# Optimization experiments

Measured on AMD Instinct MI355X. Metric: run time of the kernel, lower is better.

## Reference

```python
import jax, jax.numpy as jnp
import numpy as np

B, T = 256, 50
N_ITEMS = 100000
EMB = 256      # embedding
KBD = 128      # KBembedding == MN_dims
HID = 256      # layers[0] == layers[-1]
OUT = 256      # out_dim
NF = 10        # MN_nfactors == n_r


def setup_inputs() -> dict:
    key = jax.random.key(0)
    ks = jax.random.split(key, 18)
    s = 0.05
    return {
        "X": jax.random.randint(ks[0], (B, T), 0, N_ITEMS),
        "E": jax.random.normal(ks[1], (N_ITEMS, EMB), jnp.float32) * s,
        "KBE": jax.random.normal(ks[2], (N_ITEMS, KBD), jnp.float32) * s,
        "r_matrix": jax.random.normal(ks[3], (NF, KBD), jnp.float32) * s,
        "W_ih": jax.random.normal(ks[4], (3 * HID, EMB), jnp.float32) * s,
        "W_hh": jax.random.normal(ks[5], (3 * HID, HID), jnp.float32) * s,
        "b_ih": jnp.zeros((3 * HID,), jnp.float32),
        "b_hh": jnp.zeros((3 * HID,), jnp.float32),
        "MNu_W": jax.random.normal(ks[6], (KBD, HID), jnp.float32) * s,
        "MNu_b": jnp.zeros((KBD,), jnp.float32),
        "MNu2_W": jax.random.normal(ks[7], (HID, KBD + HID), jnp.float32) * s,
        "MNu2_b": jnp.zeros((HID,), jnp.float32),
        "MNea_W": jax.random.normal(ks[8], (KBD, KBD), jnp.float32) * s,
        "MNea_b": jnp.zeros((KBD,), jnp.float32),
        "mlp1_W": jax.random.normal(ks[9], (OUT, HID), jnp.float32) * s,
        "mlp1_b": jnp.zeros((OUT,), jnp.float32),
        "mlp2_W": jax.random.normal(ks[10], (OUT, EMB + KBD), jnp.float32) * s,
        "mlp2_b": jnp.zeros((OUT,), jnp.float32),
    }


def _gru_cell(x, h, W_ih, W_hh, b_ih, b_hh):
    # PyTorch GRUCell: gates stacked [r, z, n] along dim 0 of weights
    gi = x @ W_ih.T + b_ih
    gh = h @ W_hh.T + b_hh
    ir, iz, inn = jnp.split(gi, 3, axis=-1)
    hr, hz, hn = jnp.split(gh, 3, axis=-1)
    r = jax.nn.sigmoid(ir + hr)
    z = jax.nn.sigmoid(iz + hz)
    n = jnp.tanh(inn + r * hn)
    return (1.0 - z) * n + z * h


def reference(X, E, KBE, r_matrix, W_ih, W_hh, b_ih, b_hh,
              MNu_W, MNu_b, MNu2_W, MNu2_b, MNea_W, MNea_b,
              mlp1_W, mlp1_b, mlp2_W, mlp2_b):
    Bv, Tv = X.shape
    Em = E.at[0].set(0.0)     # mask row 0 of E
    KBm = KBE.at[0].set(0.0)  # mask row 0 of KBE
    Sx = Em[X]                # (B, T, EMB)
    KBItem = KBm[X]           # (B, T, KBD)

    def step(carry, xs):
        h, MN, y_sum = carry
        x_t, kb_t = xs                      # (B, EMB), (B, KBD)
        h = _gru_cell(x_t, h, W_ih, W_hh, b_ih, b_hh)
        y = h                                # dropout p=0 -> identity
        # gated memory write
        EA = jnp.tanh(kb_t @ MNea_W.T + MNea_b)          # (B, KBD)
        EA = EA[:, None, :] + r_matrix                    # (B, NF, KBD)
        gate = jax.nn.sigmoid(jnp.sum(MN * EA, axis=-1, keepdims=True))  # (B, NF, 1)
        MN = MN * (1.0 - gate) + EA * gate
        # attention read
        U = jnp.tanh(y @ MNu_W.T + MNu_b)                 # (B, KBD)
        AW = jax.nn.softmax(U @ r_matrix.T, axis=1)       # (B, NF)
        AC = jnp.einsum('bfd,bf->bd', MN, AW)             # (B, KBD)
        Ut = jnp.tanh(jnp.concatenate([y, AC], axis=-1) @ MNu2_W.T + MNu2_b)  # (B, HID)
        y_out = jnp.tanh(Ut @ mlp1_W.T + mlp1_b)          # (B, OUT)
        return (h, MN, y_sum + y_out), None

    init = (jnp.zeros((Bv, HID), Sx.dtype),
            jnp.zeros((Bv, NF, KBD), Sx.dtype),
            jnp.zeros((Bv, OUT), Sx.dtype))
    xs = (jnp.swapaxes(Sx, 0, 1), jnp.swapaxes(KBItem, 0, 1))  # (T, B, *)
    (h, MN, y_sum), _ = jax.lax.scan(step, init, xs)
    y = y_sum / Tv

    MergeE = jnp.concatenate([E, KBE], axis=1).at[0].set(0.0)  # (N, EMB+KBD)
    Sy = jnp.tanh(MergeE @ mlp2_W.T + mlp2_b)                  # (N, OUT)
    scores = jax.nn.log_softmax(y @ Sy.T, axis=1)              # (B, N)
    return scores, y
```

## Files before the change

kernel.cpp:

```cpp
#include <hip/hip_runtime.h>

typedef _Float16 f16;
typedef _Float16 f16x8 __attribute__((ext_vector_type(8)));
typedef float f32x4 __attribute__((ext_vector_type(4)));

#define MFMA16(a,b,c) __builtin_amdgcn_mfma_f32_16x16x32_f16(a,b,c,0,0,0)

#define NITEMS 100000
#define NBLK4  1563

#define OFF_WIH   0u
#define OFF_WHH   393216u
#define OFF_MNU   786432u
#define OFF_MNU2  851968u
#define OFF_MNEA  1048576u
#define OFF_MLP1  1081344u
#define OFF_MLP2  1212416u
#define OFF_GI    1409024u
#define OFF_TV    21069824u
#define OFF_MN    24346624u
#define OFF_YALL  57114624u
#define OFF_SY    66945024u
#define OFF_Y16   118407168u
#define OFF_PMAX  118538240u
#define OFF_PSUM  120176640u
#define OFF_LSE   121815040u

__device__ __forceinline__ float sigm(float x) { return 1.f / (1.f + __expf(-x)); }
__device__ __forceinline__ float tanh_fast(float x) {
  return 1.f - 2.f / (1.f + __expf(2.f * x));
}

__global__ __launch_bounds__(256) void k_pack(
    const float* s0, const float* s1, const float* s2, const float* s3,
    const float* s4, const float* s5, const float* s6, f16* base)
{
  int fid = blockIdx.x * 256 + threadIdx.x;
  const float* src; f16* dst; int K, f;
  if (fid < 24576)      { src = s0; dst = base;          K = 256; f = fid; }
  else if (fid < 49152) { src = s1; dst = base + 196608; K = 256; f = fid - 24576; }
  else if (fid < 53248) { src = s2; dst = base + 393216; K = 256; f = fid - 49152; }
  else if (fid < 65536) { src = s3; dst = base + 425984; K = 384; f = fid - 53248; }
  else if (fid < 67584) { src = s4; dst = base + 524288; K = 128; f = fid - 65536; }
  else if (fid < 75776) { src = s5; dst = base + 540672; K = 256; f = fid - 67584; }
  else                  { src = s6; dst = base + 606208; K = 384; f = fid - 75776; }
  int lane = f & 63, t2 = f >> 6, KS = K >> 5;
  int ks = t2 % KS, nt = t2 / KS;
  int row = nt * 16 + (lane & 15), col = ks * 32 + ((lane >> 4) << 3);
  const float* sp = src + (size_t)row * K + col;
  f16x8 v;
  #pragma unroll
  for (int j = 0; j < 8; j++) v[j] = (f16)sp[j];
  *(f16x8*)(dst + (size_t)f * 8) = v;
}

__global__ __launch_bounds__(512) void k_giea(
    const int* __restrict__ X, const float* __restrict__ E,
    const f16* __restrict__ Wih_p, const float* __restrict__ bih, f16* __restrict__ gi,
    const float* __restrict__ KBE, const f16* __restrict__ Wea_p,
    const float* __restrict__ bea, f16* __restrict__ tv)
{
  __shared__ __align__(16) f16 At[32][264];
  int tid = threadIdx.x;
  int w = tid >> 6, lane = tid & 63, lr = lane & 15, lg = lane >> 4;
  if (blockIdx.x < 400) {
    int r0 = blockIdx.x * 32;
    int t = r0 >> 8;
    {
      int r = tid >> 4, c = (tid & 15) * 16;
      int b = (r0 + r) & 255;
      int item = X[b * 50 + t];
      if (item == 0) {
        #pragma unroll
        for (int j = 0; j < 16; j++) At[r][c + j] = (f16)0.f;
      } else {
        const float4* sp = (const float4*)(E + (size_t)item * 256 + c);
        #pragma unroll
        for (int q = 0; q < 4; q++) {
          float4 v = sp[q];
          At[r][c + q*4 + 0] = (f16)v.x; At[r][c + q*4 + 1] = (f16)v.y;
          At[r][c + q*4 + 2] = (f16)v.z; At[r][c + q*4 + 3] = (f16)v.w;
        }
      }
    }
    __syncthreads();
    f32x4 acc[2][6] = {};
    for (int ks = 0; ks < 8; ks++) {
      f16x8 a0 = *(const f16x8*)(&At[lr][ks * 32 + lg * 8]);
      f16x8 a1 = *(const f16x8*)(&At[16 + lr][ks * 32 + lg * 8]);
      #pragma unroll
      for (int j = 0; j < 6; j++) {
        int nt = w * 6 + j;
        f16x8 bf = *(const f16x8*)(Wih_p + ((size_t)((nt * 8 + ks) * 64 + lane) << 3));
        acc[0][j] = MFMA16(a0, bf, acc[0][j]);
        acc[1][j] = MFMA16(a1, bf, acc[1][j]);
      }
    }
    #pragma unroll
    for (int j = 0; j < 6; j++) {
      int col = (w * 6 + j) * 16 + lr;
      float bias = bih[col];
      #pragma unroll
      for (int mt = 0; mt < 2; mt++)
        #pragma unroll
        for (int rr = 0; rr < 4; rr++) {
          int row = r0 + mt * 16 + lg * 4 + rr;
          gi[(size_t)row * 768 + col] = (f16)(acc[mt][j][rr] + bias);
        }
    }
  } else {
    int r0 = (blockIdx.x - 400) * 32;
    int t = r0 >> 8;
    {
      int r = tid >> 4, c = (tid & 15) * 8;
      int b = (r0 + r) & 255;
      int item = X[b * 50 + t];
      if (item == 0) {
        #pragma unroll
        for (int j = 0; j < 8; j++) At[r][c + j] = (f16)0.f;
      } else {
        const float4* sp = (const float4*)(KBE + (size_t)item * 128 + c);
        #pragma unroll
        for (int q = 0; q < 2; q++) {
          float4 v = sp[q];
          At[r][c + q*4 + 0] = (f16)v.x; At[r][c + q*4 + 1] = (f16)v.y;
          At[r][c + q*4 + 2] = (f16)v.z; At[r][c + q*4 + 3] = (f16)v.w;
        }
      }
    }
    __syncthreads();
    f32x4 acc[2] = {};
    for (int ks = 0; ks < 4; ks++) {
      f16x8 a0 = *(const f16x8*)(&At[lr][ks * 32 + lg * 8]);
      f16x8 a1 = *(const f16x8*)(&At[16 + lr][ks * 32 + lg * 8]);
      f16x8 bf = *(const f16x8*)(Wea_p + ((size_t)((w * 4 + ks) * 64 + lane) << 3));
      acc[0] = MFMA16(a0, bf, acc[0]);
      acc[1] = MFMA16(a1, bf, acc[1]);
    }
    int col = w * 16 + lr;
    float bias = bea[col];
    #pragma unroll
    for (int mt = 0; mt < 2; mt++)
      #pragma unroll
      for (int rr = 0; rr < 4; rr++) {
        int row = r0 + mt * 16 + lg * 4 + rr;
        tv[(size_t)row * 128 + col] = (f16)tanh_fast(acc[mt][rr] + bias);
      }
  }
}

__global__ __launch_bounds__(1024)
__attribute__((amdgpu_waves_per_eu(4, 4)))
void k_fused(
    const f16* __restrict__ Whh_p, const float* __restrict__ bhh,
    const f16* __restrict__ gi, f16* __restrict__ y_all,
    const f16* __restrict__ tv, const float* __restrict__ Rm, f16* __restrict__ MN,
    const float* __restrict__ E, const float* __restrict__ KBE,
    const f16* __restrict__ mlp2_p, const float* __restrict__ mlp2b, f16* __restrict__ Sy)
{
  __shared__ __align__(16) char smem[147456];
  int tid = threadIdx.x, w = tid >> 6, lane = tid & 63, lr = lane & 15, lg = lane >> 4;

  if (blockIdx.x < 32) {
    f16* Wlds = (f16*)smem;
    f16* hb0 = (f16*)(smem + 131072);
    f16* hb1 = (f16*)(smem + 139264);
    int r0 = blockIdx.x * 8;
    {
      const float4* src = (const float4*)Whh_p;
      float4* dst = (float4*)Wlds;
      #pragma unroll
      for (int i = 0; i < 8; i++) dst[tid + i * 1024] = src[tid + i * 1024];
      float4 z4 = {0.f, 0.f, 0.f, 0.f};
      ((float4*)hb0)[tid] = z4;
    }
    f16x8 Wz[8], Wn[8];
    #pragma unroll
    for (int ks = 0; ks < 8; ks++) {
      Wz[ks] = *(const f16x8*)(Whh_p + ((size_t)(((16 + w) * 8 + ks) * 64 + lane) << 3));
      Wn[ks] = *(const f16x8*)(Whh_p + ((size_t)(((32 + w) * 8 + ks) * 64 + lane) << 3));
      asm volatile("" : "+a"(Wz[ks]), "+a"(Wn[ks]));
    }
    int col = w * 16 + lr;
    float bR = bhh[col], bZ = bhh[col + 256], bN = bhh[col + 512];
    float hreg[4] = {0.f, 0.f, 0.f, 0.f};
    const f16* gP = gi + (size_t)(r0 + lg * 4) * 768 + col;
    f16 P[4][3];
    if (lg < 2) {
      #pragma unroll
      for (int rr = 0; rr < 4; rr++)
        #pragma unroll
        for (int g = 0; g < 3; g++)
          P[rr][g] = gP[rr * 768 + g * 256];
    }
    __syncthreads();
    f16* hc = hb0; f16* hn_ = hb1;
    int xr = (lr & 7) << 4;
    const f16* wB0 = Wlds + (size_t)w * 4096 + lane * 8;
    for (int t = 0; t < 50; t++) {
      f32x4 aR = {}, aZ = {}, aN = {};
      const char* hbase = (const char*)hc + lr * 512;
      #pragma unroll
      for (int ks = 0; ks < 8; ks++) {
        f16x8 a = *(const f16x8*)(hbase + ((ks * 64 + lg * 16) ^ xr));
        aR = MFMA16(a, *(const f16x8*)(wB0 + ks * 512), aR);
        aZ = MFMA16(a, Wz[ks], aZ);
        aN = MFMA16(a, Wn[ks], aN);
      }
      if (lg < 2) {
        #pragma unroll
        for (int rr = 0; rr < 4; rr++) {
          int row = lg * 4 + rr;
          float rg = sigm((float)P[rr][0] + aR[rr] + bR);
          float zg = sigm((float)P[rr][1] + aZ[rr] + bZ);
          float ng = tanh_fast((float)P[rr][2] + rg * (aN[rr] + bN));
          float hv = ng + zg * (hreg[rr] - ng);
          hreg[rr] = hv;
          *(f16*)((char*)hn_ + row * 512 + ((col * 2) ^ ((row & 7) << 4))) = (f16)hv;
        }
        if (t < 49) {
          const f16* gN = gP + (size_t)(t + 1) * 196608;
          #pragma unroll
          for (int rr = 0; rr < 4; rr++)
            #pragma unroll
            for (int g = 0; g < 3; g++)
              P[rr][g] = gN[rr * 768 + g * 256];
        }
      }
      __syncthreads();
      if (tid < 256) {
        int row = tid >> 5, c = tid & 31;
        f16x8 hv = *(const f16x8*)((char*)hn_ + row * 512 + ((c * 16) ^ ((row & 7) << 4)));
        *(f16x8*)(y_all + ((size_t)t * 256 + r0 + row) * 256 + c * 8) = hv;
      }
      f16* tmp = hc; hc = hn_; hn_ = tmp;
    }
  } else if (blockIdx.x < 192) {
    int pair = (blockIdx.x - 32) * 16 + w;
    int b = pair / 10, f = pair - (pair / 10) * 10;
    float r0_ = Rm[f * 128 + lane], r1_ = Rm[f * 128 + 64 + lane];
    float mn0 = 0.f, mn1 = 0.f;
    for (int t = 0; t < 50; t++) {
      size_t base = ((size_t)t * 256 + b) * 128;
      float ea0 = (float)tv[base + lane] + r0_;
      float ea1 = (float)tv[base + 64 + lane] + r1_;
      float p = mn0 * ea0 + mn1 * ea1;
      #pragma unroll
      for (int off = 32; off > 0; off >>= 1) p += __shfl_xor(p, off);
      float g = sigm(p);
      mn0 += (ea0 - mn0) * g;
      mn1 += (ea1 - mn1) * g;
      size_t mb = (((size_t)t * 256 + b) * 10 + f) * 128;
      MN[mb + lane] = (f16)mn0;
      MN[mb + 64 + lane] = (f16)mn1;
    }
  } else {
    f16* At = (f16*)smem;
    int i0 = (blockIdx.x - 192) * 32;
    {
      int r = tid >> 5;
      int item = i0 + r;
      int c = (tid & 31) * 8;
      if (item == 0) {
        #pragma unroll
        for (int j = 0; j < 8; j++) At[r * 392 + c + j] = (f16)0.f;
      } else {
        const float4* sp = (const float4*)(E + (size_t)item * 256 + c);
        #pragma unroll
        for (int q = 0; q < 2; q++) {
          float4 v = sp[q];
          At[r * 392 + c + q*4 + 0] = (f16)v.x; At[r * 392 + c + q*4 + 1] = (f16)v.y;
          At[r * 392 + c + q*4 + 2] = (f16)v.z; At[r * 392 + c + q*4 + 3] = (f16)v.w;
        }
      }
      int c2 = (tid & 31) * 4;
      if (item == 0) {
        #pragma unroll
        for (int j = 0; j < 4; j++) At[r * 392 + 256 + c2 + j] = (f16)0.f;
      } else {
        float4 v = *(const float4*)(KBE + (size_t)item * 128 + c2);
        At[r * 392 + 256 + c2 + 0] = (f16)v.x; At[r * 392 + 256 + c2 + 1] = (f16)v.y;
        At[r * 392 + 256 + c2 + 2] = (f16)v.z; At[r * 392 + 256 + c2 + 3] = (f16)v.w;
      }
    }
    __syncthreads();
    int mt = w & 1, ntp = w >> 1;
    f32x4 acc[2] = {};
    for (int ks = 0; ks < 12; ks++) {
      f16x8 a = *(const f16x8*)(&At[(mt * 16 + lr) * 392 + ks * 32 + lg * 8]);
      #pragma unroll
      for (int j = 0; j < 2; j++) {
        int nt = ntp * 2 + j;
        f16x8 bf = *(const f16x8*)(mlp2_p + ((size_t)((nt * 12 + ks) * 64 + lane) << 3));
        acc[j] = MFMA16(a, bf, acc[j]);
      }
    }
    #pragma unroll
    for (int j = 0; j < 2; j++) {
      int col = (ntp * 2 + j) * 16 + lr;
      float bias = mlp2b[col];
      #pragma unroll
      for (int rr = 0; rr < 4; rr++) {
        int item = i0 + mt * 16 + lg * 4 + rr;
        Sy[(size_t)item * 256 + col] = (f16)tanh_fast(acc[j][rr] + bias);
      }
    }
  }
}

__global__ __launch_bounds__(512) void k_uacut(
    const f16* __restrict__ y_all, const f16* __restrict__ MNu_p,
    const float* __restrict__ MNub, const float* __restrict__ Rm,
    const f16* __restrict__ MN,
    const f16* __restrict__ MNu2_p, const float* __restrict__ MNu2b,
    const f16* __restrict__ mlp1_p, const float* __restrict__ mlp1b,
    float* __restrict__ ypart)
{
  __shared__ __align__(16) char smem[25088];
  int tid = threadIdx.x, w = tid >> 6, lane = tid & 63, lr = lane & 15, lg = lane >> 4;
  f16   (*Aty)[264] = (f16(*)[264])smem;
  float (*Uf)[136]  = (float(*)[136])(smem + 8448);
  f16   (*Utl)[264] = (f16(*)[264])(smem + 8448);
  float (*Lg)[10]   = (float(*)[10])(smem + 17152);
  float (*Aw)[10]   = (float(*)[10])(smem + 17792);
  f16   (*ACs)[136] = (f16(*)[136])(smem + 18432);
  int r0 = blockIdx.x * 16;
  {
    int r = tid >> 5, c = (tid & 31) * 8;
    f16x8 v = *(const f16x8*)(y_all + (size_t)(r0 + r) * 256 + c);
    *(f16x8*)(&Aty[r][c]) = v;
  }
  __syncthreads();
  {
    f32x4 acc = {};
    for (int ks = 0; ks < 8; ks++) {
      f16x8 a = *(const f16x8*)(&Aty[lr][ks * 32 + lg * 8]);
      f16x8 bf = *(const f16x8*)(MNu_p + ((size_t)((w * 8 + ks) * 64 + lane) << 3));
      acc = MFMA16(a, bf, acc);
    }
    int col = w * 16 + lr;
    float bias = MNub[col];
    #pragma unroll
    for (int rr = 0; rr < 4; rr++)
      Uf[lg * 4 + rr][col] = tanh_fast(acc[rr] + bias);
  }
  __syncthreads();
  if (tid < 160) {
    int row = tid / 10, f = tid - (tid / 10) * 10;
    float s = 0.f;
    for (int d = 0; d < 128; d++) s += Uf[row][d] * Rm[f * 128 + d];
    Lg[row][f] = s;
  }
  __syncthreads();
  if (tid < 16) {
    float m = -1e30f;
    #pragma unroll
    for (int f = 0; f < 10; f++) m = fmaxf(m, Lg[tid][f]);
    float e[10], s = 0.f;
    #pragma unroll
    for (int f = 0; f < 10; f++) { e[f] = __expf(Lg[tid][f] - m); s += e[f]; }
    float inv = 1.f / s;
    #pragma unroll
    for (int f = 0; f < 10; f++) Aw[tid][f] = e[f] * inv;
  }
  __syncthreads();
  if (tid < 256) {
    int row = tid >> 4, d0 = (tid & 15) * 8;
    float a[8] = {0,0,0,0,0,0,0,0};
    for (int f = 0; f < 10; f++) {
      float wgt = Aw[row][f];
      f16x8 mv = *(const f16x8*)(MN + (((size_t)(r0 + row)) * 10 + f) * 128 + d0);
      #pragma unroll
      for (int q = 0; q < 8; q++) a[q] += wgt * (float)mv[q];
    }
    f16x8 o;
    #pragma unroll
    for (int q = 0; q < 8; q++) o[q] = (f16)a[q];
    *(f16x8*)(&ACs[row][d0]) = o;
  }
  __syncthreads();
  {
    f32x4 acc[2] = {};
    for (int ks = 0; ks < 12; ks++) {
      f16x8 a = (ks < 8)
        ? *(const f16x8*)(&Aty[lr][ks * 32 + lg * 8])
        : *(const f16x8*)(&ACs[lr][(ks - 8) * 32 + lg * 8]);
      #pragma unroll
      for (int j = 0; j < 2; j++) {
        f16x8 bf = *(const f16x8*)(MNu2_p + ((size_t)(((w * 2 + j) * 12 + ks) * 64 + lane) << 3));
        acc[j] = MFMA16(a, bf, acc[j]);
      }
    }
    __syncthreads();
    #pragma unroll
    for (int j = 0; j < 2; j++) {
      int col = (w * 2 + j) * 16 + lr;
      float bias = MNu2b[col];
      #pragma unroll
      for (int rr = 0; rr < 4; rr++)
        Utl[lg * 4 + rr][col] = (f16)tanh_fast(acc[j][rr] + bias);
    }
  }
  __syncthreads();
  {
    f32x4 acc2[2] = {};
    for (int ks = 0; ks < 8; ks++) {
      f16x8 a = *(const f16x8*)(&Utl[lr][ks * 32 + lg * 8]);
      #pragma unroll
      for (int j = 0; j < 2; j++) {
        f16x8 bf = *(const f16x8*)(mlp1_p + ((size_t)(((w * 2 + j) * 8 + ks) * 64 + lane) << 3));
        acc2[j] = MFMA16(a, bf, acc2[j]);
      }
    }
    #pragma unroll
    for (int j = 0; j < 2; j++) {
      int col = (w * 2 + j) * 16 + lr;
      float bias = mlp1b[col];
      #pragma unroll
      for (int rr = 0; rr < 4; rr++) {
        int row = r0 + lg * 4 + rr;
        ypart[(size_t)row * 256 + col] = tanh_fast(acc2[j][rr] + bias);
      }
    }
  }
}

__global__ __launch_bounds__(256) void k_yfin(
    const float* __restrict__ ypart, float* __restrict__ outy, f16* __restrict__ y16)
{
  int b = blockIdx.x, c = threadIdx.x;
  float s = 0.f;
  for (int t = 0; t < 50; t++) s += ypart[((size_t)t * 256 + b) * 256 + c];
  float v = s * (1.0f / 50.0f);
  outy[b * 256 + c] = v;
  y16[b * 256 + c] = (f16)v;
}

template <int FINAL>
__global__ __launch_bounds__(512) void k_scores(
    const f16* __restrict__ y16, const f16* __restrict__ Sy,
    const float* __restrict__ lse, float* __restrict__ pmax,
    float* __restrict__ psum, float* __restrict__ out)
{
  __shared__ __align__(16) char smx[FINAL ? 67584 : 4096];
  int tid = threadIdx.x, w = tid >> 6, lane = tid & 63, lr = lane & 15, lg = lane >> 4;
  int i0 = blockIdx.x * 64;
  int mtb = (w >> 1) * 4, ntb = (w & 1) * 2;
  f32x4 acc[4][2] = {};
  for (int ks = 0; ks < 8; ks++) {
    f16x8 a[4];
    #pragma unroll
    for (int i = 0; i < 4; i++)
      a[i] = *(const f16x8*)(y16 + ((size_t)((mtb + i) * 16 + lr)) * 256 + ks * 32 + lg * 8);
    #pragma unroll
    for (int j = 0; j < 2; j++) {
      int item = i0 + (ntb + j) * 16 + lr;
      int ic = item < NITEMS ? item : (NITEMS - 1);
      f16x8 bv = *(const f16x8*)(Sy + (size_t)ic * 256 + ks * 32 + lg * 8);
      #pragma unroll
      for (int i = 0; i < 4; i++) acc[i][j] = MFMA16(a[i], bv, acc[i][j]);
    }
  }
  if constexpr (!FINAL) {
    float* pm = (float*)smx;
    float* ps = (float*)(smx + 2048);
    int item0 = i0 + ntb * 16 + lr, item1 = item0 + 16;
    bool v0 = item0 < NITEMS, v1 = item1 < NITEMS;
    #pragma unroll
    for (int i = 0; i < 4; i++)
      #pragma unroll
      for (int rr = 0; rr < 4; rr++) {
        float x0 = v0 ? acc[i][0][rr] : -1e30f;
        float x1 = v1 ? acc[i][1][rr] : -1e30f;
        float m = fmaxf(x0, x1);
        m = fmaxf(m, __shfl_xor(m, 1)); m = fmaxf(m, __shfl_xor(m, 2));
        m = fmaxf(m, __shfl_xor(m, 4)); m = fmaxf(m, __shfl_xor(m, 8));
        float s = (v0 ? __expf(x0 - m) : 0.f) + (v1 ? __expf(x1 - m) : 0.f);
        s += __shfl_xor(s, 1); s += __shfl_xor(s, 2);
        s += __shfl_xor(s, 4); s += __shfl_xor(s, 8);
        if (lr == 0) {
          int row = (mtb + i) * 16 + lg * 4 + rr;
          pm[(w & 1) * 256 + row] = m;
          ps[(w & 1) * 256 + row] = s;
        }
      }
    __syncthreads();
    if (tid < 256) {
      float m0 = pm[tid], m1 = pm[256 + tid];
      float s0 = ps[tid], s1 = ps[256 + tid];
      float M = fmaxf(m0, m1);
      float S = s0 * __expf(m0 - M) + s1 * __expf(m1 - M);
      pmax[(size_t)tid * 1600 + blockIdx.x] = M;
      psum[(size_t)tid * 1600 + blockIdx.x] = S;
    }
  } else {
    float (*oS)[65] = (float(*)[65])smx;
    float* lse_s = (float*)(smx + 66560);
    if (tid < 256) lse_s[tid] = lse[tid];
    __syncthreads();
    #pragma unroll
    for (int i = 0; i < 4; i++)
      #pragma unroll
      for (int j = 0; j < 2; j++)
        #pragma unroll
        for (int rr = 0; rr < 4; rr++) {
          int row = (mtb + i) * 16 + lg * 4 + rr;
          int c = (ntb + j) * 16 + lr;
          oS[row][c] = acc[i][j][rr] - lse_s[row];
        }
    __syncthreads();
    for (int it = 0; it < 32; it++) {
      int row = it * 8 + (tid >> 6);
      int c = tid & 63;
      if (i0 + c < NITEMS) out[(size_t)row * NITEMS + i0 + c] = oS[row][c];
    }
  }
}

__global__ __launch_bounds__(256) void k_lse(
    const float* __restrict__ pmax, const float* __restrict__ psum, float* __restrict__ lse)
{
  int b = blockIdx.x, tid = threadIdx.x;
  __shared__ float red[256];
  float m = -1e30f;
  for (int i = tid; i < NBLK4; i += 256) m = fmaxf(m, pmax[(size_t)b * 1600 + i]);
  red[tid] = m; __syncthreads();
  for (int s = 128; s > 0; s >>= 1) {
    if (tid < s) red[tid] = fmaxf(red[tid], red[tid + s]);
    __syncthreads();
  }
  float M = red[0]; __syncthreads();
  float s = 0.f;
  for (int i = tid; i < NBLK4; i += 256)
    s += psum[(size_t)b * 1600 + i] * __expf(pmax[(size_t)b * 1600 + i] - M);
  red[tid] = s; __syncthreads();
  for (int q = 128; q > 0; q >>= 1) {
    if (tid < q) red[tid] += red[tid + q];
    __syncthreads();
  }
  if (tid == 0) lse[b] = M + logf(red[0]);
}

extern "C" void kernel_launch(void* const* d_in, const int* in_sizes, int n_in,
                              void* d_out, int out_size, void* d_ws, size_t ws_size,
                              hipStream_t stream) {
  (void)in_sizes; (void)n_in; (void)out_size; (void)ws_size;
  const int*   X     = (const int*)d_in[0];
  const float* E     = (const float*)d_in[1];
  const float* KBE   = (const float*)d_in[2];
  const float* Rm    = (const float*)d_in[3];
  const float* Wih   = (const float*)d_in[4];
  const float* Whh   = (const float*)d_in[5];
  const float* bih   = (const float*)d_in[6];
  const float* bhh   = (const float*)d_in[7];
  const float* MNuW  = (const float*)d_in[8];
  const float* MNub  = (const float*)d_in[9];
  const float* MNu2W = (const float*)d_in[10];
  const float* MNu2b = (const float*)d_in[11];
  const float* MNeaW = (const float*)d_in[12];
  const float* MNeab = (const float*)d_in[13];
  const float* mlp1W = (const float*)d_in[14];
  const float* mlp1b = (const float*)d_in[15];
  const float* mlp2W = (const float*)d_in[16];
  const float* mlp2b = (const float*)d_in[17];

  char* ws = (char*)d_ws;
  f16*   Wih_p  = (f16*)(ws + OFF_WIH);
  f16*   Whh_p  = (f16*)(ws + OFF_WHH);
  f16*   MNu_p  = (f16*)(ws + OFF_MNU);
  f16*   MNu2_p = (f16*)(ws + OFF_MNU2);
  f16*   Wea_p  = (f16*)(ws + OFF_MNEA);
  f16*   mlp1_p = (f16*)(ws + OFF_MLP1);
  f16*   mlp2_p = (f16*)(ws + OFF_MLP2);
  f16*   gi     = (f16*)(ws + OFF_GI);
  f16*   tv     = (f16*)(ws + OFF_TV);
  f16*   MN     = (f16*)(ws + OFF_MN);
  f16*   y_all  = (f16*)(ws + OFF_YALL);
  f16*   Sy     = (f16*)(ws + OFF_SY);
  float* ypart  = (float*)(ws + OFF_GI);
  f16*   y16    = (f16*)(ws + OFF_Y16);
  float* pmax   = (float*)(ws + OFF_PMAX);
  float* psum   = (float*)(ws + OFF_PSUM);
  float* lse    = (float*)(ws + OFF_LSE);
  float* outf   = (float*)d_out;

  k_pack<<<344, 256, 0, stream>>>(Wih, Whh, MNuW, MNu2W, MNeaW, mlp1W, mlp2W, (f16*)ws);
  k_giea<<<800, 512, 0, stream>>>(X, E, Wih_p, bih, gi, KBE, Wea_p, MNeab, tv);
  k_fused<<<3317, 1024, 0, stream>>>(Whh_p, bhh, gi, y_all, tv, Rm, MN,
                                     E, KBE, mlp2_p, mlp2b, Sy);
  k_uacut<<<800, 512, 0, stream>>>(y_all, MNu_p, MNub, Rm, MN,
                                   MNu2_p, MNu2b, mlp1_p, mlp1b, ypart);
  k_yfin<<<256, 256, 0, stream>>>(ypart, outf + 25600000, y16);
  k_scores<0><<<NBLK4, 512, 0, stream>>>(y16, Sy, nullptr, pmax, psum, nullptr);
  k_lse<<<256, 256, 0, stream>>>(pmax, psum, lse);
  k_scores<1><<<NBLK4, 512, 0, stream>>>(y16, Sy, lse, nullptr, nullptr, outf);
}
```

Measured before the change: 382.4 us.

## Stream GRU weights from global, prefetch MN inputs, drop LDS staging in score writeout

The GRU recurrence stops pinning the z and n weight fragments in registers and reloads them from global (L2-cached) memory at every step. The MN update loop prefetches the next timestep's tv values one step ahead. The final score kernel is split out of the template and writes scores directly from MFMA accumulators to global memory instead of transposing through a 66KB LDS tile. This frees registers and LDS, raising occupancy, at the cost of less coalesced output stores and extra global weight traffic inside the serial GRU loop.

```diff
diff --git a/kernel.cpp b/kernel.cpp
--- a/kernel.cpp
+++ b/kernel.cpp
@@ -174,13 +174,6 @@
       float4 z4 = {0.f, 0.f, 0.f, 0.f};
       ((float4*)hb0)[tid] = z4;
     }
-    f16x8 Wz[8], Wn[8];
-    #pragma unroll
-    for (int ks = 0; ks < 8; ks++) {
-      Wz[ks] = *(const f16x8*)(Whh_p + ((size_t)(((16 + w) * 8 + ks) * 64 + lane) << 3));
-      Wn[ks] = *(const f16x8*)(Whh_p + ((size_t)(((32 + w) * 8 + ks) * 64 + lane) << 3));
-      asm volatile("" : "+a"(Wz[ks]), "+a"(Wn[ks]));
-    }
     int col = w * 16 + lr;
     float bR = bhh[col], bZ = bhh[col + 256], bN = bhh[col + 512];
     float hreg[4] = {0.f, 0.f, 0.f, 0.f};
@@ -197,6 +190,8 @@
     f16* hc = hb0; f16* hn_ = hb1;
     int xr = (lr & 7) << 4;
     const f16* wB0 = Wlds + (size_t)w * 4096 + lane * 8;
+    const f16* wBz = Whh_p + ((size_t)((16 + w) * 8) * 64 + lane) * 8;
+    const f16* wBn = Whh_p + ((size_t)((32 + w) * 8) * 64 + lane) * 8;
     for (int t = 0; t < 50; t++) {
       f32x4 aR = {}, aZ = {}, aN = {};
       const char* hbase = (const char*)hc + lr * 512;
@@ -204,8 +199,8 @@
       for (int ks = 0; ks < 8; ks++) {
         f16x8 a = *(const f16x8*)(hbase + ((ks * 64 + lg * 16) ^ xr));
         aR = MFMA16(a, *(const f16x8*)(wB0 + ks * 512), aR);
-        aZ = MFMA16(a, Wz[ks], aZ);
-        aN = MFMA16(a, Wn[ks], aN);
+        aZ = MFMA16(a, *(const f16x8*)(wBz + ks * 512), aZ);
+        aN = MFMA16(a, *(const f16x8*)(wBn + ks * 512), aN);
       }
       if (lg < 2) {
         #pragma unroll
@@ -240,10 +235,16 @@
     int b = pair / 10, f = pair - (pair / 10) * 10;
     float r0_ = Rm[f * 128 + lane], r1_ = Rm[f * 128 + 64 + lane];
     float mn0 = 0.f, mn1 = 0.f;
+    float c0 = (float)tv[(size_t)b * 128 + lane];
+    float c1 = (float)tv[(size_t)b * 128 + 64 + lane];
     for (int t = 0; t < 50; t++) {
-      size_t base = ((size_t)t * 256 + b) * 128;
-      float ea0 = (float)tv[base + lane] + r0_;
-      float ea1 = (float)tv[base + 64 + lane] + r1_;
+      float ea0 = c0 + r0_;
+      float ea1 = c1 + r1_;
+      if (t < 49) {
+        size_t nb = ((size_t)(t + 1) * 256 + b) * 128;
+        c0 = (float)tv[nb + lane];
+        c1 = (float)tv[nb + 64 + lane];
+      }
       float p = mn0 * ea0 + mn1 * ea1;
       #pragma unroll
       for (int off = 32; off > 0; off >>= 1) p += __shfl_xor(p, off);
@@ -436,13 +437,11 @@
   y16[b * 256 + c] = (f16)v;
 }
 
-template <int FINAL>
-__global__ __launch_bounds__(512) void k_scores(
+__global__ __launch_bounds__(512) void k_score0(
     const f16* __restrict__ y16, const f16* __restrict__ Sy,
-    const float* __restrict__ lse, float* __restrict__ pmax,
-    float* __restrict__ psum, float* __restrict__ out)
-{
-  __shared__ __align__(16) char smx[FINAL ? 67584 : 4096];
+    float* __restrict__ pmax, float* __restrict__ psum)
+{
+  __shared__ float pm[512], ps[512];
   int tid = threadIdx.x, w = tid >> 6, lane = tid & 63, lr = lane & 15, lg = lane >> 4;
   int i0 = blockIdx.x * 64;
   int mtb = (w >> 1) * 4, ntb = (w & 1) * 2;
@@ -461,9 +460,7 @@
       for (int i = 0; i < 4; i++) acc[i][j] = MFMA16(a[i], bv, acc[i][j]);
     }
   }
-  if constexpr (!FINAL) {
-    float* pm = (float*)smx;
-    float* ps = (float*)(smx + 2048);
+  {
     int item0 = i0 + ntb * 16 + lr, item1 = item0 + 16;
     bool v0 = item0 < NITEMS, v1 = item1 < NITEMS;
     #pragma unroll
@@ -484,36 +481,15 @@
           ps[(w & 1) * 256 + row] = s;
         }
       }
-    __syncthreads();
-    if (tid < 256) {
-      float m0 = pm[tid], m1 = pm[256 + tid];
-      float s0 = ps[tid], s1 = ps[256 + tid];
-      float M = fmaxf(m0, m1);
-      float S = s0 * __expf(m0 - M) + s1 * __expf(m1 - M);
-      pmax[(size_t)tid * 1600 + blockIdx.x] = M;
-      psum[(size_t)tid * 1600 + blockIdx.x] = S;
-    }
-  } else {
-    float (*oS)[65] = (float(*)[65])smx;
-    float* lse_s = (float*)(smx + 66560);
-    if (tid < 256) lse_s[tid] = lse[tid];
-    __syncthreads();
-    #pragma unroll
-    for (int i = 0; i < 4; i++)
-      #pragma unroll
-      for (int j = 0; j < 2; j++)
-        #pragma unroll
-        for (int rr = 0; rr < 4; rr++) {
-          int row = (mtb + i) * 16 + lg * 4 + rr;
-          int c = (ntb + j) * 16 + lr;
-          oS[row][c] = acc[i][j][rr] - lse_s[row];
-        }
-    __syncthreads();
-    for (int it = 0; it < 32; it++) {
-      int row = it * 8 + (tid >> 6);
-      int c = tid & 63;
-      if (i0 + c < NITEMS) out[(size_t)row * NITEMS + i0 + c] = oS[row][c];
-    }
+  }
+  __syncthreads();
+  if (tid < 256) {
+    float m0 = pm[tid], m1 = pm[256 + tid];
+    float s0 = ps[tid], s1 = ps[256 + tid];
+    float M = fmaxf(m0, m1);
+    float S = s0 * __expf(m0 - M) + s1 * __expf(m1 - M);
+    pmax[(size_t)tid * 1600 + blockIdx.x] = M;
+    psum[(size_t)tid * 1600 + blockIdx.x] = S;
   }
 }
 
@@ -539,6 +515,46 @@
     __syncthreads();
   }
   if (tid == 0) lse[b] = M + logf(red[0]);
+}
+
+__global__ __launch_bounds__(512) void k_scores1(
+    const f16* __restrict__ y16, const f16* __restrict__ Sy,
+    const float* __restrict__ lse, float* __restrict__ out)
+{
+  __shared__ float lse_s[256];
+  int tid = threadIdx.x, w = tid >> 6, lane = tid & 63, lr = lane & 15, lg = lane >> 4;
+  if (tid < 256) lse_s[tid] = lse[tid];
+  int i0 = blockIdx.x * 64;
+  int mtb = (w >> 1) * 4, ntb = (w & 1) * 2;
+  f32x4 acc[4][2] = {};
+  for (int ks = 0; ks < 8; ks++) {
+    f16x8 a[4];
+    #pragma unroll
+    for (int i = 0; i < 4; i++)
+      a[i] = *(const f16x8*)(y16 + ((size_t)((mtb + i) * 16 + lr)) * 256 + ks * 32 + lg * 8);
+    #pragma unroll
+    for (int j = 0; j < 2; j++) {
+      int item = i0 + (ntb + j) * 16 + lr;
+      int ic = item < NITEMS ? item : (NITEMS - 1);
+      f16x8 bv = *(const f16x8*)(Sy + (size_t)ic * 256 + ks * 32 + lg * 8);
+      #pragma unroll
+      for (int i = 0; i < 4; i++) acc[i][j] = MFMA16(a[i], bv, acc[i][j]);
+    }
+  }
+  __syncthreads();
+  #pragma unroll
+  for (int i = 0; i < 4; i++)
+    #pragma unroll
+    for (int j = 0; j < 2; j++) {
+      int c = i0 + (ntb + j) * 16 + lr;
+      if (c < NITEMS) {
+        #pragma unroll
+        for (int rr = 0; rr < 4; rr++) {
+          int row = (mtb + i) * 16 + lg * 4 + rr;
+          out[(size_t)row * NITEMS + c] = acc[i][j][rr] - lse_s[row];
+        }
+      }
+    }
 }
 
 extern "C" void kernel_launch(void* const* d_in, const int* in_sizes, int n_in,
@@ -591,7 +607,7 @@
   k_uacut<<<800, 512, 0, stream>>>(y_all, MNu_p, MNub, Rm, MN,
                                    MNu2_p, MNu2b, mlp1_p, mlp1b, ypart);
   k_yfin<<<256, 256, 0, stream>>>(ypart, outf + 25600000, y16);
-  k_scores<0><<<NBLK4, 512, 0, stream>>>(y16, Sy, nullptr, pmax, psum, nullptr);
+  k_score0<<<NBLK4, 512, 0, stream>>>(y16, Sy, pmax, psum);
   k_lse<<<256, 256, 0, stream>>>(pmax, psum, lse);
-  k_scores<1><<<NBLK4, 512, 0, stream>>>(y16, Sy, lse, nullptr, nullptr, outf);
-}
+  k_scores1<<<NBLK4, 512, 0, stream>>>(y16, Sy, lse, outf);
+}
```

Result: faster. 374.8 us (-2.0%).
